# Kernel optimization log

Hardware: AMD Instinct MI355X
Metric: run time of the kernel (lower is better)

Reference implementation:

```python
import jax, jax.numpy as jnp
import numpy as np

B, N_CLASS, N_CENTER, HIDDEN = 1024, 50, 8, 512
INIT_MU, BETA, EPS = 0.1, 0.5, 1e-8


def setup_inputs() -> dict:
    key = jax.random.key(0)
    k1, k2, k3, k4 = jax.random.split(key, 4)
    x = jax.random.normal(k1, (B, HIDDEN), dtype=jnp.float32)
    # class_mu ~ U(-init_mu, init_mu), matching torch.rand(...) * 2*init_mu - init_mu
    class_mu = jax.random.uniform(k2, (N_CLASS, N_CENTER, HIDDEN),
                                  minval=-INIT_MU, maxval=INIT_MU, dtype=jnp.float32)
    # binary dropout-style mask: (rand > beta).float()
    mask = (jax.random.uniform(k3, (N_CENTER, HIDDEN)) > BETA).astype(jnp.float32)
    # fixed random projection W ~ 0.1 * N(0,1)
    W = jax.random.normal(k4, (HIDDEN, HIDDEN), dtype=jnp.float32) * 0.1
    return {"x": x, "class_mu": class_mu, "mask": mask, "W": W}


def reference(x, class_mu, mask, W):
    # [B, n_center, hidden]: per-center masked copy of x, then shared projection W
    masked = x[:, None, :] * mask[None, :, :]
    mul = jnp.einsum('bch,hd->bcd', masked, W)
    # broadcast squared-distance against cluster centers: [B, n_class, n_center]
    diff = mul[:, None, :, :] - class_mu[None, :, :, :]  # [B, K, C, H]
    score = 1.0 / (1.0 + jnp.sum(diff * diff, axis=-1))  # Student-t style kernel
    # normalize over n_center (dim 2)
    distances = score / (jnp.sum(score, axis=2, keepdims=True) + EPS)
    # k_assign: second normalization over last dim (n_center)
    k_assign = distances / jnp.sum(distances, axis=-1, keepdims=True)
    return (mul, k_assign, distances)
```

## Files before the change

kernel.cpp:

```cpp
#include <hip/hip_runtime.h>

typedef short s16x8 __attribute__((ext_vector_type(8)));
typedef float f32x4 __attribute__((ext_vector_type(4)));

#define NB      1024
#define NCLASS  50
#define NCENTER 8
#define HID     512
#define KPAD    64
#define MROWS   8192

#define OFF_ABF    0u
#define OFF_WT     8388608u
#define OFF_MUBF   8912896u
#define OFF_MUNORM 9437184u
#define OFF_MULBF  9439232u
#define OFF_SCORE  17827840u

#define OUT_KA 4194304
#define OUT_D  4603904

__device__ __forceinline__ short f2bf(float f) {
    unsigned int u = __float_as_uint(f);
    unsigned int r = (u + 0x7FFFu + ((u >> 16) & 1u)) >> 16;
    return (short)(unsigned short)r;
}
__device__ __forceinline__ float bf2f(short h) {
    return __uint_as_float(((unsigned int)(unsigned short)h) << 16);
}

__global__ __launch_bounds__(256) void prep_kernel(
    const float* __restrict__ x, const float* __restrict__ class_mu,
    const float* __restrict__ mask, const float* __restrict__ W,
    short* __restrict__ Abf, short* __restrict__ WT,
    short* __restrict__ Mubf, float* __restrict__ Munorm)
{
    __shared__ float lds[64][65];
    const int blk = blockIdx.x, tid = threadIdx.x;

    if (blk < 256) {
        #pragma unroll
        for (int i = 0; i < 8; ++i) {
            int g = (blk * 256 + tid) + i * 65536;
            int e = g * 8;
            int r = e >> 9;
            int k = e & 511;
            int b = r >> 3, c = r & 7;
            const float4* xp = (const float4*)(x + b * HID + k);
            const float4* mp = (const float4*)(mask + c * HID + k);
            float4 x0 = xp[0], x1 = xp[1];
            float4 m0 = mp[0], m1 = mp[1];
            s16x8 o;
            o[0] = f2bf(x0.x * m0.x); o[1] = f2bf(x0.y * m0.y);
            o[2] = f2bf(x0.z * m0.z); o[3] = f2bf(x0.w * m0.w);
            o[4] = f2bf(x1.x * m1.x); o[5] = f2bf(x1.y * m1.y);
            o[6] = f2bf(x1.z * m1.z); o[7] = f2bf(x1.w * m1.w);
            *(s16x8*)(Abf + e) = o;
        }
    } else if (blk < 320) {
        int t = blk - 256;
        int th = t & 7, td = t >> 3;
        int col = tid & 63, rb = tid >> 6;
        #pragma unroll
        for (int it = 0; it < 16; ++it) {
            int row = it * 4 + rb;
            lds[row][col] = W[(th * 64 + row) * HID + td * 64 + col];
        }
        __syncthreads();
        #pragma unroll
        for (int it = 0; it < 16; ++it) {
            int row = it * 4 + rb;
            WT[(td * 64 + row) * HID + th * 64 + col] = f2bf(lds[col][row]);
        }
    } else {
        int w = (blk - 320) * 4 + (tid >> 6);
        int lane = tid & 63;
        int c = w >> 6, kk = w & 63;
        int h = lane * 8;
        float v[8];
        if (kk < NCLASS) {
            const float4* p = (const float4*)(class_mu + (kk * NCENTER + c) * HID + h);
            float4 a = p[0], bq = p[1];
            v[0] = a.x;  v[1] = a.y;  v[2] = a.z;  v[3] = a.w;
            v[4] = bq.x; v[5] = bq.y; v[6] = bq.z; v[7] = bq.w;
        } else {
            #pragma unroll
            for (int j = 0; j < 8; ++j) v[j] = 0.f;
        }
        s16x8 o; float sq = 0.f;
        #pragma unroll
        for (int j = 0; j < 8; ++j) { o[j] = f2bf(v[j]); sq += v[j] * v[j]; }
        *(s16x8*)(Mubf + (c * KPAD + kk) * HID + h) = o;
        sq += __shfl_xor(sq, 1);  sq += __shfl_xor(sq, 2);  sq += __shfl_xor(sq, 4);
        sq += __shfl_xor(sq, 8);  sq += __shfl_xor(sq, 16); sq += __shfl_xor(sq, 32);
        if (lane == 0) Munorm[c * KPAD + kk] = sq;
    }
}

__global__ __launch_bounds__(256) void gemm_mul(
    const short* __restrict__ Abf, const short* __restrict__ WT,
    float* __restrict__ mul_out, short* __restrict__ mulbf)
{
    __shared__ short As[128 * 32];
    __shared__ short Bs[128 * 32];
    const int tid = threadIdx.x;
    const int bm = blockIdx.x * 128;
    const int bn = blockIdx.y * 128;
    const int wave = tid >> 6, lane = tid & 63;
    const int wm = (wave & 1) * 64, wn = (wave >> 1) * 64;
    const int q = lane >> 4, l16 = lane & 15;

    f32x4 acc[4][4] = {};

    const int r0 = tid >> 2, c0 = (tid & 3) * 8;

    for (int it = 0; it < 16; ++it) {
        const int k0 = it * 32;
        *(s16x8*)(As + r0 * 32 + c0)        = *(const s16x8*)(Abf + (bm + r0) * HID + k0 + c0);
        *(s16x8*)(As + (r0 + 64) * 32 + c0) = *(const s16x8*)(Abf + (bm + r0 + 64) * HID + k0 + c0);
        *(s16x8*)(Bs + r0 * 32 + c0)        = *(const s16x8*)(WT + (bn + r0) * HID + k0 + c0);
        *(s16x8*)(Bs + (r0 + 64) * 32 + c0) = *(const s16x8*)(WT + (bn + r0 + 64) * HID + k0 + c0);
        __syncthreads();

        s16x8 af[4], bfr[4];
        #pragma unroll
        for (int mt = 0; mt < 4; ++mt)
            af[mt] = *(const s16x8*)(As + (wm + mt * 16 + l16) * 32 + q * 8);
        #pragma unroll
        for (int nt = 0; nt < 4; ++nt)
            bfr[nt] = *(const s16x8*)(Bs + (wn + nt * 16 + l16) * 32 + q * 8);
        #pragma unroll
        for (int mt = 0; mt < 4; ++mt)
            #pragma unroll
            for (int nt = 0; nt < 4; ++nt)
                acc[mt][nt] = __builtin_amdgcn_mfma_f32_16x16x32_bf16(af[mt], bfr[nt], acc[mt][nt], 0, 0, 0);
        __syncthreads();
    }

    #pragma unroll
    for (int mt = 0; mt < 4; ++mt) {
        #pragma unroll
        for (int nt = 0; nt < 4; ++nt) {
            #pragma unroll
            for (int reg = 0; reg < 4; ++reg) {
                int gr = bm + wm + mt * 16 + q * 4 + reg;
                int gc = bn + wn + nt * 16 + l16;
                float v = acc[mt][nt][reg];
                mul_out[gr * HID + gc] = v;
                mulbf[gr * HID + gc] = f2bf(v);
            }
        }
    }
}

__global__ __launch_bounds__(128) void score_kernel(
    const short* __restrict__ mulbf, const short* __restrict__ Mubf,
    const float* __restrict__ Munorm, float* __restrict__ score)
{
    const int tid = threadIdx.x;
    const int c = blockIdx.x & 7, bt = blockIdx.x >> 3;
    const int wave = tid >> 6, lane = tid & 63;
    const int q = lane >> 4, l16 = lane & 15;
    const int b0 = bt * 32 + wave * 16;

    f32x4 acc[4] = {};
    float nrm = 0.f;

    const short* arow = mulbf + ((b0 + l16) * NCENTER + c) * HID + q * 8;
    const short* brow = Mubf + (c * KPAD + l16) * HID + q * 8;

    for (int it = 0; it < 16; ++it) {
        const int k0 = it * 32;
        s16x8 av  = *(const s16x8*)(arow + k0);
        s16x8 bv0 = *(const s16x8*)(brow + k0);
        s16x8 bv1 = *(const s16x8*)(brow + 16 * HID + k0);
        s16x8 bv2 = *(const s16x8*)(brow + 32 * HID + k0);
        s16x8 bv3 = *(const s16x8*)(brow + 48 * HID + k0);
        #pragma unroll
        for (int j = 0; j < 8; ++j) { float f = bf2f(av[j]); nrm += f * f; }
        acc[0] = __builtin_amdgcn_mfma_f32_16x16x32_bf16(av, bv0, acc[0], 0, 0, 0);
        acc[1] = __builtin_amdgcn_mfma_f32_16x16x32_bf16(av, bv1, acc[1], 0, 0, 0);
        acc[2] = __builtin_amdgcn_mfma_f32_16x16x32_bf16(av, bv2, acc[2], 0, 0, 0);
        acc[3] = __builtin_amdgcn_mfma_f32_16x16x32_bf16(av, bv3, acc[3], 0, 0, 0);
    }

    nrm += __shfl_xor(nrm, 16);
    nrm += __shfl_xor(nrm, 32);
    float rowNorm[4];
    #pragma unroll
    for (int reg = 0; reg < 4; ++reg) rowNorm[reg] = __shfl(nrm, q * 4 + reg);

    #pragma unroll
    for (int nt = 0; nt < 4; ++nt) {
        float mn = Munorm[c * KPAD + nt * 16 + l16];
        #pragma unroll
        for (int reg = 0; reg < 4; ++reg) {
            float sq = rowNorm[reg] + mn - 2.f * acc[nt][reg];
            float sc = 1.f / (1.f + sq);
            int b = b0 + q * 4 + reg;
            int kcls = nt * 16 + l16;
            score[(b * KPAD + kcls) * NCENTER + c] = sc;
        }
    }
}

__global__ __launch_bounds__(256) void norm_kernel(
    const float* __restrict__ score, float* __restrict__ out)
{
    int t = blockIdx.x * 256 + threadIdx.x;
    if (t >= NB * NCLASS) return;
    int b = t / NCLASS, k = t % NCLASS;
    const float4* sp = (const float4*)(score + (b * KPAD + k) * NCENTER);
    float4 s0 = sp[0], s1 = sp[1];
    float S = s0.x + s0.y + s0.z + s0.w + s1.x + s1.y + s1.z + s1.w;
    float invd = 1.f / (S + 1e-8f);
    float invk = 1.f / S;
    float4 ka0, ka1, dd0, dd1;
    ka0.x = s0.x * invk; ka0.y = s0.y * invk; ka0.z = s0.z * invk; ka0.w = s0.w * invk;
    ka1.x = s1.x * invk; ka1.y = s1.y * invk; ka1.z = s1.z * invk; ka1.w = s1.w * invk;
    dd0.x = s0.x * invd; dd0.y = s0.y * invd; dd0.z = s0.z * invd; dd0.w = s0.w * invd;
    dd1.x = s1.x * invd; dd1.y = s1.y * invd; dd1.z = s1.z * invd; dd1.w = s1.w * invd;
    float* kap = out + OUT_KA + (b * NCLASS + k) * NCENTER;
    float* dp  = out + OUT_D  + (b * NCLASS + k) * NCENTER;
    ((float4*)kap)[0] = ka0; ((float4*)kap)[1] = ka1;
    ((float4*)dp)[0]  = dd0; ((float4*)dp)[1]  = dd1;
}

extern "C" void kernel_launch(void* const* d_in, const int* in_sizes, int n_in,
                              void* d_out, int out_size, void* d_ws, size_t ws_size,
                              hipStream_t stream) {
    const float* x        = (const float*)d_in[0];
    const float* class_mu = (const float*)d_in[1];
    const float* mask     = (const float*)d_in[2];
    const float* W        = (const float*)d_in[3];
    float* out = (float*)d_out;
    char* ws = (char*)d_ws;

    short* Abf    = (short*)(ws + OFF_ABF);
    short* WT     = (short*)(ws + OFF_WT);
    short* Mubf   = (short*)(ws + OFF_MUBF);
    float* Munorm = (float*)(ws + OFF_MUNORM);
    short* mulbf  = (short*)(ws + OFF_MULBF);
    float* score  = (float*)(ws + OFF_SCORE);

    prep_kernel<<<448, 256, 0, stream>>>(x, class_mu, mask, W, Abf, WT, Mubf, Munorm);
    gemm_mul<<<dim3(64, 4), 256, 0, stream>>>(Abf, WT, out, mulbf);
    score_kernel<<<256, 128, 0, stream>>>(mulbf, Mubf, Munorm, score);
    norm_kernel<<<200, 256, 0, stream>>>(score, out);
}
```

Before: 98.06 us.

## Fuse masking into GEMM, fuse score and normalization, drop intermediate buffers

The masked bf16 A-matrix is no longer materialized. The GEMM loads x and mask directly, converts them in registers, and prefetches the next k-slice before the LDS store. The GEMM tile shrinks to 64 rows so twice as many blocks are launched. The separate bf16 copy of mul is removed, and the score kernel reads fp32 mul and converts it itself. The score and normalization kernels are merged through an LDS tile, which removes the score scratch round trip and one launch, at the cost of more redundant global reads of x, mask and mul.

```diff
diff --git a/kernel.cpp b/kernel.cpp
--- a/kernel.cpp
+++ b/kernel.cpp
@@ -8,14 +8,10 @@
 #define NCENTER 8
 #define HID     512
 #define KPAD    64
-#define MROWS   8192
-
-#define OFF_ABF    0u
-#define OFF_WT     8388608u
-#define OFF_MUBF   8912896u
-#define OFF_MUNORM 9437184u
-#define OFF_MULBF  9439232u
-#define OFF_SCORE  17827840u
+
+#define OFF_WT     0u
+#define OFF_MUBF   524288u
+#define OFF_MUNORM 1048576u
 
 #define OUT_KA 4194304
 #define OUT_D  4603904
@@ -25,41 +21,16 @@
     unsigned int r = (u + 0x7FFFu + ((u >> 16) & 1u)) >> 16;
     return (short)(unsigned short)r;
 }
-__device__ __forceinline__ float bf2f(short h) {
-    return __uint_as_float(((unsigned int)(unsigned short)h) << 16);
-}
 
 __global__ __launch_bounds__(256) void prep_kernel(
-    const float* __restrict__ x, const float* __restrict__ class_mu,
-    const float* __restrict__ mask, const float* __restrict__ W,
-    short* __restrict__ Abf, short* __restrict__ WT,
-    short* __restrict__ Mubf, float* __restrict__ Munorm)
+    const float* __restrict__ class_mu, const float* __restrict__ W,
+    short* __restrict__ WT, short* __restrict__ Mubf, float* __restrict__ Munorm)
 {
     __shared__ float lds[64][65];
     const int blk = blockIdx.x, tid = threadIdx.x;
 
-    if (blk < 256) {
-        #pragma unroll
-        for (int i = 0; i < 8; ++i) {
-            int g = (blk * 256 + tid) + i * 65536;
-            int e = g * 8;
-            int r = e >> 9;
-            int k = e & 511;
-            int b = r >> 3, c = r & 7;
-            const float4* xp = (const float4*)(x + b * HID + k);
-            const float4* mp = (const float4*)(mask + c * HID + k);
-            float4 x0 = xp[0], x1 = xp[1];
-            float4 m0 = mp[0], m1 = mp[1];
-            s16x8 o;
-            o[0] = f2bf(x0.x * m0.x); o[1] = f2bf(x0.y * m0.y);
-            o[2] = f2bf(x0.z * m0.z); o[3] = f2bf(x0.w * m0.w);
-            o[4] = f2bf(x1.x * m1.x); o[5] = f2bf(x1.y * m1.y);
-            o[6] = f2bf(x1.z * m1.z); o[7] = f2bf(x1.w * m1.w);
-            *(s16x8*)(Abf + e) = o;
-        }
-    } else if (blk < 320) {
-        int t = blk - 256;
-        int th = t & 7, td = t >> 3;
+    if (blk < 64) {
+        int th = blk & 7, td = blk >> 3;
         int col = tid & 63, rb = tid >> 6;
         #pragma unroll
         for (int it = 0; it < 16; ++it) {
@@ -73,7 +44,7 @@
             WT[(td * 64 + row) * HID + th * 64 + col] = f2bf(lds[col][row]);
         }
     } else {
-        int w = (blk - 320) * 4 + (tid >> 6);
+        int w = (blk - 64) * 4 + (tid >> 6);
         int lane = tid & 63;
         int c = w >> 6, kk = w & 63;
         int h = lane * 8;
@@ -98,132 +69,139 @@
 }
 
 __global__ __launch_bounds__(256) void gemm_mul(
-    const short* __restrict__ Abf, const short* __restrict__ WT,
-    float* __restrict__ mul_out, short* __restrict__ mulbf)
+    const float* __restrict__ x, const float* __restrict__ mask,
+    const short* __restrict__ WT, float* __restrict__ mul_out)
 {
-    __shared__ short As[128 * 32];
+    __shared__ short As[64 * 32];
     __shared__ short Bs[128 * 32];
     const int tid = threadIdx.x;
-    const int bm = blockIdx.x * 128;
+    const int bm = blockIdx.x * 64;
     const int bn = blockIdx.y * 128;
     const int wave = tid >> 6, lane = tid & 63;
-    const int wm = (wave & 1) * 64, wn = (wave >> 1) * 64;
+    const int wm = (wave & 1) * 32, wn = (wave >> 1) * 64;
     const int q = lane >> 4, l16 = lane & 15;
 
-    f32x4 acc[4][4] = {};
+    f32x4 acc[2][4] = {};
 
     const int r0 = tid >> 2, c0 = (tid & 3) * 8;
-
+    const int xr = (bm >> 3) + (r0 >> 3);
+    const float* xp = x + xr * HID + c0;
+    const float* mp = mask + (r0 & 7) * HID + c0;
+    const short* wp = WT + (bn + r0) * HID + c0;
+
+    float4 xa, xb, ma, mb; s16x8 w0, w1;
+#define GLOAD(IT) do { const int kq = (IT) * 32; \
+        xa = *(const float4*)(xp + kq); xb = *(const float4*)(xp + kq + 4); \
+        ma = *(const float4*)(mp + kq); mb = *(const float4*)(mp + kq + 4); \
+        w0 = *(const s16x8*)(wp + kq);  w1 = *(const s16x8*)(wp + 64 * HID + kq); } while (0)
+
+    GLOAD(0);
+    #pragma unroll
     for (int it = 0; it < 16; ++it) {
-        const int k0 = it * 32;
-        *(s16x8*)(As + r0 * 32 + c0)        = *(const s16x8*)(Abf + (bm + r0) * HID + k0 + c0);
-        *(s16x8*)(As + (r0 + 64) * 32 + c0) = *(const s16x8*)(Abf + (bm + r0 + 64) * HID + k0 + c0);
-        *(s16x8*)(Bs + r0 * 32 + c0)        = *(const s16x8*)(WT + (bn + r0) * HID + k0 + c0);
-        *(s16x8*)(Bs + (r0 + 64) * 32 + c0) = *(const s16x8*)(WT + (bn + r0 + 64) * HID + k0 + c0);
+        s16x8 oa;
+        oa[0] = f2bf(xa.x * ma.x); oa[1] = f2bf(xa.y * ma.y);
+        oa[2] = f2bf(xa.z * ma.z); oa[3] = f2bf(xa.w * ma.w);
+        oa[4] = f2bf(xb.x * mb.x); oa[5] = f2bf(xb.y * mb.y);
+        oa[6] = f2bf(xb.z * mb.z); oa[7] = f2bf(xb.w * mb.w);
+        s16x8 cw0 = w0, cw1 = w1;
+        if (it < 15) GLOAD(it + 1);
+
         __syncthreads();
-
-        s16x8 af[4], bfr[4];
-        #pragma unroll
-        for (int mt = 0; mt < 4; ++mt)
+        *(s16x8*)(As + r0 * 32 + c0)        = oa;
+        *(s16x8*)(Bs + r0 * 32 + c0)        = cw0;
+        *(s16x8*)(Bs + (r0 + 64) * 32 + c0) = cw1;
+        __syncthreads();
+
+        s16x8 af[2], bfr[4];
+        #pragma unroll
+        for (int mt = 0; mt < 2; ++mt)
             af[mt] = *(const s16x8*)(As + (wm + mt * 16 + l16) * 32 + q * 8);
         #pragma unroll
         for (int nt = 0; nt < 4; ++nt)
             bfr[nt] = *(const s16x8*)(Bs + (wn + nt * 16 + l16) * 32 + q * 8);
         #pragma unroll
-        for (int mt = 0; mt < 4; ++mt)
+        for (int mt = 0; mt < 2; ++mt)
             #pragma unroll
             for (int nt = 0; nt < 4; ++nt)
                 acc[mt][nt] = __builtin_amdgcn_mfma_f32_16x16x32_bf16(af[mt], bfr[nt], acc[mt][nt], 0, 0, 0);
-        __syncthreads();
-    }
+    }
+#undef GLOAD
 
     #pragma unroll
-    for (int mt = 0; mt < 4; ++mt) {
-        #pragma unroll
-        for (int nt = 0; nt < 4; ++nt) {
+    for (int mt = 0; mt < 2; ++mt)
+        #pragma unroll
+        for (int nt = 0; nt < 4; ++nt)
             #pragma unroll
             for (int reg = 0; reg < 4; ++reg) {
                 int gr = bm + wm + mt * 16 + q * 4 + reg;
                 int gc = bn + wn + nt * 16 + l16;
-                float v = acc[mt][nt][reg];
-                mul_out[gr * HID + gc] = v;
-                mulbf[gr * HID + gc] = f2bf(v);
+                mul_out[gr * HID + gc] = acc[mt][nt][reg];
             }
-        }
-    }
-}
-
-__global__ __launch_bounds__(128) void score_kernel(
-    const short* __restrict__ mulbf, const short* __restrict__ Mubf,
-    const float* __restrict__ Munorm, float* __restrict__ score)
+}
+
+__global__ __launch_bounds__(512) void score_norm_kernel(
+    const float* __restrict__ mul, const short* __restrict__ Mubf,
+    const float* __restrict__ Munorm, float* __restrict__ out)
 {
+    __shared__ float sc[16][16][9];
     const int tid = threadIdx.x;
-    const int c = blockIdx.x & 7, bt = blockIdx.x >> 3;
-    const int wave = tid >> 6, lane = tid & 63;
+    const int bt = blockIdx.x >> 2, kt = blockIdx.x & 3;
+    const int b0 = bt * 16, kbase = kt * 16;
+    const int c = tid >> 6;
+    const int lane = tid & 63;
     const int q = lane >> 4, l16 = lane & 15;
-    const int b0 = bt * 32 + wave * 16;
-
-    f32x4 acc[4] = {};
+
+    f32x4 acc = {};
     float nrm = 0.f;
 
-    const short* arow = mulbf + ((b0 + l16) * NCENTER + c) * HID + q * 8;
-    const short* brow = Mubf + (c * KPAD + l16) * HID + q * 8;
-
+    const float* arow = mul + ((b0 + l16) * NCENTER + c) * HID + q * 8;
+    const short* brow = Mubf + (c * KPAD + kbase + l16) * HID + q * 8;
+
+    #pragma unroll 4
     for (int it = 0; it < 16; ++it) {
         const int k0 = it * 32;
-        s16x8 av  = *(const s16x8*)(arow + k0);
-        s16x8 bv0 = *(const s16x8*)(brow + k0);
-        s16x8 bv1 = *(const s16x8*)(brow + 16 * HID + k0);
-        s16x8 bv2 = *(const s16x8*)(brow + 32 * HID + k0);
-        s16x8 bv3 = *(const s16x8*)(brow + 48 * HID + k0);
-        #pragma unroll
-        for (int j = 0; j < 8; ++j) { float f = bf2f(av[j]); nrm += f * f; }
-        acc[0] = __builtin_amdgcn_mfma_f32_16x16x32_bf16(av, bv0, acc[0], 0, 0, 0);
-        acc[1] = __builtin_amdgcn_mfma_f32_16x16x32_bf16(av, bv1, acc[1], 0, 0, 0);
-        acc[2] = __builtin_amdgcn_mfma_f32_16x16x32_bf16(av, bv2, acc[2], 0, 0, 0);
-        acc[3] = __builtin_amdgcn_mfma_f32_16x16x32_bf16(av, bv3, acc[3], 0, 0, 0);
+        float4 a0 = *(const float4*)(arow + k0);
+        float4 a1 = *(const float4*)(arow + k0 + 4);
+        s16x8 bv = *(const s16x8*)(brow + k0);
+        s16x8 av;
+        av[0] = f2bf(a0.x); av[1] = f2bf(a0.y); av[2] = f2bf(a0.z); av[3] = f2bf(a0.w);
+        av[4] = f2bf(a1.x); av[5] = f2bf(a1.y); av[6] = f2bf(a1.z); av[7] = f2bf(a1.w);
+        nrm += a0.x * a0.x + a0.y * a0.y + a0.z * a0.z + a0.w * a0.w
+             + a1.x * a1.x + a1.y * a1.y + a1.z * a1.z + a1.w * a1.w;
+        acc = __builtin_amdgcn_mfma_f32_16x16x32_bf16(av, bv, acc, 0, 0, 0);
     }
 
     nrm += __shfl_xor(nrm, 16);
     nrm += __shfl_xor(nrm, 32);
-    float rowNorm[4];
+
+    float mn = Munorm[c * KPAD + kbase + l16];
     #pragma unroll
-    for (int reg = 0; reg < 4; ++reg) rowNorm[reg] = __shfl(nrm, q * 4 + reg);
-
-    #pragma unroll
-    for (int nt = 0; nt < 4; ++nt) {
-        float mn = Munorm[c * KPAD + nt * 16 + l16];
-        #pragma unroll
-        for (int reg = 0; reg < 4; ++reg) {
-            float sq = rowNorm[reg] + mn - 2.f * acc[nt][reg];
-            float sc = 1.f / (1.f + sq);
-            int b = b0 + q * 4 + reg;
-            int kcls = nt * 16 + l16;
-            score[(b * KPAD + kcls) * NCENTER + c] = sc;
-        }
-    }
-}
-
-__global__ __launch_bounds__(256) void norm_kernel(
-    const float* __restrict__ score, float* __restrict__ out)
-{
-    int t = blockIdx.x * 256 + threadIdx.x;
-    if (t >= NB * NCLASS) return;
-    int b = t / NCLASS, k = t % NCLASS;
-    const float4* sp = (const float4*)(score + (b * KPAD + k) * NCENTER);
-    float4 s0 = sp[0], s1 = sp[1];
-    float S = s0.x + s0.y + s0.z + s0.w + s1.x + s1.y + s1.z + s1.w;
-    float invd = 1.f / (S + 1e-8f);
-    float invk = 1.f / S;
-    float4 ka0, ka1, dd0, dd1;
-    ka0.x = s0.x * invk; ka0.y = s0.y * invk; ka0.z = s0.z * invk; ka0.w = s0.w * invk;
-    ka1.x = s1.x * invk; ka1.y = s1.y * invk; ka1.z = s1.z * invk; ka1.w = s1.w * invk;
-    dd0.x = s0.x * invd; dd0.y = s0.y * invd; dd0.z = s0.z * invd; dd0.w = s0.w * invd;
-    dd1.x = s1.x * invd; dd1.y = s1.y * invd; dd1.z = s1.z * invd; dd1.w = s1.w * invd;
-    float* kap = out + OUT_KA + (b * NCLASS + k) * NCENTER;
-    float* dp  = out + OUT_D  + (b * NCLASS + k) * NCENTER;
-    ((float4*)kap)[0] = ka0; ((float4*)kap)[1] = ka1;
-    ((float4*)dp)[0]  = dd0; ((float4*)dp)[1]  = dd1;
+    for (int reg = 0; reg < 4; ++reg) {
+        float rn = __shfl(nrm, q * 4 + reg);
+        float sq = rn + mn - 2.f * acc[reg];
+        sc[q * 4 + reg][l16][c] = 1.f / (1.f + sq);
+    }
+    __syncthreads();
+
+    if (tid < 256) {
+        int b = tid >> 4, k = tid & 15;
+        int kcls = kbase + k;
+        if (kcls < NCLASS) {
+            float s0 = sc[b][k][0], s1 = sc[b][k][1], s2 = sc[b][k][2], s3 = sc[b][k][3];
+            float s4 = sc[b][k][4], s5 = sc[b][k][5], s6 = sc[b][k][6], s7 = sc[b][k][7];
+            float S = ((s0 + s1) + (s2 + s3)) + ((s4 + s5) + (s6 + s7));
+            float invd = 1.f / (S + 1e-8f);
+            float invk = 1.f / S;
+            float* kap = out + OUT_KA + ((b0 + b) * NCLASS + kcls) * NCENTER;
+            float* dp  = out + OUT_D  + ((b0 + b) * NCLASS + kcls) * NCENTER;
+            float4 ka0 = {s0 * invk, s1 * invk, s2 * invk, s3 * invk};
+            float4 ka1 = {s4 * invk, s5 * invk, s6 * invk, s7 * invk};
+            float4 dd0 = {s0 * invd, s1 * invd, s2 * invd, s3 * invd};
+            float4 dd1 = {s4 * invd, s5 * invd, s6 * invd, s7 * invd};
+            ((float4*)kap)[0] = ka0; ((float4*)kap)[1] = ka1;
+            ((float4*)dp)[0]  = dd0; ((float4*)dp)[1]  = dd1;
+        }
+    }
 }
 
 extern "C" void kernel_launch(void* const* d_in, const int* in_sizes, int n_in,
@@ -236,15 +214,11 @@
     float* out = (float*)d_out;
     char* ws = (char*)d_ws;
 
-    short* Abf    = (short*)(ws + OFF_ABF);
     short* WT     = (short*)(ws + OFF_WT);
     short* Mubf   = (short*)(ws + OFF_MUBF);
     float* Munorm = (float*)(ws + OFF_MUNORM);
-    short* mulbf  = (short*)(ws + OFF_MULBF);
-    float* score  = (float*)(ws + OFF_SCORE);
-
-    prep_kernel<<<448, 256, 0, stream>>>(x, class_mu, mask, W, Abf, WT, Mubf, Munorm);
-    gemm_mul<<<dim3(64, 4), 256, 0, stream>>>(Abf, WT, out, mulbf);
-    score_kernel<<<256, 128, 0, stream>>>(mulbf, Mubf, Munorm, score);
-    norm_kernel<<<200, 256, 0, stream>>>(score, out);
-}
+
+    prep_kernel<<<192, 256, 0, stream>>>(class_mu, W, WT, Mubf, Munorm);
+    gemm_mul<<<dim3(128, 4), 256, 0, stream>>>(x, mask, WT, out);
+    score_norm_kernel<<<256, 512, 0, stream>>>(out, Mubf, Munorm, out);
+}
```

After: 93.68 us. -4.5%, faster.
